# Kernel tuning notes

Hardware: AMD Instinct MI355X
Metric: run time of the kernel (lower is better)

The kernel has to match this reference:

```python
import jax, jax.numpy as jnp
import numpy as np

B, SQ, SK, D = 8, 2048, 2048, 128


def setup_inputs() -> dict:
    key = jax.random.key(0)
    kq, kk, kv = jax.random.split(key, 3)
    Q = jax.random.normal(kq, (B, SQ, D), dtype=jnp.float32)
    K = jax.random.normal(kk, (B, SK, D), dtype=jnp.float32)
    V = jax.random.normal(kv, (B, SK, D), dtype=jnp.float32)
    return {"Q": Q, "K": K, "V": V}


def reference(Q, K, V):
    d_k = K.shape[2]  # NOTE: module divides by d_k, not sqrt(d_k)
    # scores: [B, Sq, Sk]
    scores = jnp.einsum('bqd,bkd->bqk', Q, K) / d_k
    # unconventional softmax over the batch dim (dim=0), as in the source
    attn = jax.nn.softmax(scores, axis=0)
    # output: [B, Sq, D]
    return jnp.einsum('bqk,bkd->bqd', attn, V)
```

## Files before the change

kernel.cpp:

```cpp
#include <hip/hip_runtime.h>
#include <hip/hip_bf16.h>

#define B_   8
#define SQ_  2048
#define SK_  2048
#define D_   128

typedef __attribute__((ext_vector_type(8))) _Float16 f16x8;
typedef __attribute__((ext_vector_type(4))) _Float16 f16x4;
typedef __attribute__((ext_vector_type(4))) float    f32x4;

#define QK_BSTRIDE (128 * 4 * 64 * 8)
#define VF_BSTRIDE (64 * 8 * 64 * 8)

__device__ __forceinline__ void dma16(const void* g, void* l) {
    __builtin_amdgcn_global_load_lds(
        (const __attribute__((address_space(1))) unsigned int*)g,
        (__attribute__((address_space(3))) unsigned int*)l, 16, 0, 0);
}

__global__ __launch_bounds__(256)
void qkprep(const float* __restrict__ Q, const float* __restrict__ K,
            _Float16* __restrict__ Qf, _Float16* __restrict__ Kf) {
    const float* src = blockIdx.y ? K : Q;
    _Float16*    dst = blockIdx.y ? Kf : Qf;
    int gid = blockIdx.x * 256 + threadIdx.x;
    int l  = gid & 63;
    int ks = (gid >> 6) & 3;
    int t  = (gid >> 8) & 127;
    int b  = gid >> 15;
    const float* p = src + ((size_t)b * 2048 + t * 16 + (l & 15)) * 128
                         + ks * 32 + (l >> 4) * 8;
    f32x4 a = *(const f32x4*)p;
    f32x4 c = *(const f32x4*)(p + 4);
    f16x8 r;
    r[0] = (_Float16)a[0]; r[1] = (_Float16)a[1];
    r[2] = (_Float16)a[2]; r[3] = (_Float16)a[3];
    r[4] = (_Float16)c[0]; r[5] = (_Float16)c[1];
    r[6] = (_Float16)c[2]; r[7] = (_Float16)c[3];
    *(f16x8*)(dst + (size_t)gid * 8) = r;
}

__global__ __launch_bounds__(256)
void vprep(const float* __restrict__ V, _Float16* __restrict__ Vf) {
    __shared__ _Float16 T[64][136];
    const int b  = blockIdx.y;
    const int kb = blockIdx.x;
    const int t  = threadIdx.x;
    const int row = t >> 2, c0 = (t & 3) * 32;
    const float* src = V + ((size_t)b * SK_ + kb * 64 + row) * D_ + c0;
#pragma unroll
    for (int u = 0; u < 8; ++u) {
        f32x4 v = *(const f32x4*)(src + u * 4);
        f16x4 h;
        h[0] = (_Float16)v[0]; h[1] = (_Float16)v[1];
        h[2] = (_Float16)v[2]; h[3] = (_Float16)v[3];
        *(f16x4*)&T[row][c0 + u * 4] = h;
    }
    __syncthreads();
#pragma unroll
    for (int u = 0; u < 4; ++u) {
        int s   = u * 256 + t;
        int l   = s & 63;
        int dt  = (s >> 6) & 7;
        int ktl = s >> 9;
        int hi  = l >> 4, ql = l & 15;
        f16x8 r;
#pragma unroll
        for (int j = 0; j < 8; ++j) r[j] = T[ktl * 32 + hi * 8 + j][dt * 16 + ql];
        *(f16x8*)(Vf + (((size_t)b * 64 + kb * 2 + ktl) * 8 + dt) * 512 + (size_t)l * 8) = r;
    }
}

__global__ __launch_bounds__(512)
void zred(const _Float16* __restrict__ Qf, const _Float16* __restrict__ Kf,
          _Float16* __restrict__ Pf, int nqt, int qoff16) {
    __shared__ __attribute__((aligned(16))) _Float16 E[8][64][64];
    const int bid   = blockIdx.x;
    const int qtile = bid >> 5;
    const int ktile = bid & 31;
    const int b  = threadIdx.x >> 6;
    const int l  = threadIdx.x & 63;
    const int hi = l >> 4, ql = l & 15;

    const _Float16* Qb = Qf + (size_t)b * QK_BSTRIDE;
    const _Float16* Kb = Kf + (size_t)b * QK_BSTRIDE;

    f32x4 s[4][4] = {};
#pragma unroll
    for (int ks = 0; ks < 4; ++ks) {
        f16x8 kf[4];
#pragma unroll
        for (int kk = 0; kk < 4; ++kk)
            kf[kk] = *(const f16x8*)(Kb + ((((size_t)ktile * 4 + kk) * 4 + ks) * 64 + l) * 8);
#pragma unroll
        for (int qq = 0; qq < 4; ++qq) {
            f16x8 qv = *(const f16x8*)(Qb + ((((size_t)(qoff16 + qtile * 4 + qq)) * 4 + ks) * 64 + l) * 8);
#pragma unroll
            for (int kk = 0; kk < 4; ++kk)
                s[kk][qq] = __builtin_amdgcn_mfma_f32_16x16x32_f16(kf[kk], qv, s[kk][qq], 0, 0, 0);
        }
    }

    f16x4* E4 = (f16x4*)&E[0][0][0];
#pragma unroll
    for (int kk = 0; kk < 4; ++kk)
#pragma unroll
        for (int qq = 0; qq < 4; ++qq) {
            f16x4 e;
#pragma unroll
            for (int r = 0; r < 4; ++r)
                e[r] = (_Float16)__expf(s[kk][qq][r] * 0.0078125f);
            int q = qq * 16 + ql;
            int k = kk * 16 + hi * 4;
            int g16 = ((b * 64 + q) << 3) + ((k >> 3) ^ (q & 7));
            E4[g16 * 2 + ((k >> 2) & 1)] = e;
        }
    __syncthreads();

    const int t    = threadIdx.x;
    const int ktl  = t >> 8;
    const int qq2  = (t >> 6) & 3;
    const int l2   = t & 63;
    const int hi2  = l2 >> 4, ql2 = l2 & 15;
    const int q_loc  = qq2 * 16 + ql2;
    const int k0_loc = ktl * 32 + hi2 * 8;
    const f16x8* E8  = (const f16x8*)&E[0][0][0];
    const int eidx   = (q_loc << 3) + ((k0_loc >> 3) ^ (q_loc & 7));

    f16x8 z = E8[eidx];
#pragma unroll
    for (int bb = 1; bb < 8; ++bb) z = z + E8[bb * 512 + eidx];
    float inv[8];
#pragma unroll
    for (int j = 0; j < 8; ++j) inv[j] = __builtin_amdgcn_rcpf((float)z[j]);

    const size_t pbase = (((size_t)(qtile * 4 + qq2)) * 64 + (ktile * 2 + ktl)) * 512 + (size_t)l2 * 8;
#pragma unroll
    for (int bb = 0; bb < 8; ++bb) {
        f16x8 e = E8[bb * 512 + eidx];
        f16x8 p;
#pragma unroll
        for (int j = 0; j < 8; ++j) p[j] = (_Float16)((float)e[j] * inv[j]);
        *(f16x8*)(Pf + (size_t)bb * nqt * 32768 + pbase) = p;
    }
}

__global__ __launch_bounds__(512)
void av(const _Float16* __restrict__ Pf, const _Float16* __restrict__ Vf,
        float* __restrict__ out, int nqt, int qoff) {
    __shared__ __attribute__((aligned(16))) _Float16 lds[2 * 12288];

    const int bid = blockIdx.x;
    const int b   = bid & 7;
    const int mt  = bid >> 3;
    const int w   = threadIdx.x >> 6;
    const int l   = threadIdx.x & 63;
    const int wq  = w >> 2;
    const int wd  = w & 3;
    const int hi  = l >> 4, ql = l & 15;

    const _Float16* Pb = Pf + (size_t)b * nqt * 32768;
    const _Float16* Vb = Vf + (size_t)b * VF_BSTRIDE;

#define STAGE(bufi, kt2) do {                                                  \
    _Float16* dst0 = (_Float16*)lds + (bufi) * 12288;                          \
    _Pragma("unroll")                                                          \
    for (int u = 0; u < 3; ++u) {                                              \
        int c = w * 3 + u;                                                     \
        const _Float16* srcp;                                                  \
        if (c < 8)                                                             \
            srcp = Pb + (((size_t)(mt * 4 + (c >> 1))) * 64 + ((kt2) * 2 + (c & 1))) * 512 + (size_t)l * 8; \
        else {                                                                 \
            int cv = c - 8;                                                    \
            srcp = Vb + (((size_t)((kt2) * 2 + (cv >> 3))) * 8 + (cv & 7)) * 512 + (size_t)l * 8; \
        }                                                                      \
        dma16(srcp, dst0 + c * 512);                                           \
    }                                                                          \
} while (0)

    f32x4 acc[2][2] = {};
    int cur = 0;
    STAGE(0, 0);
    for (int kt2 = 0; kt2 < 32; ++kt2) {
        if (kt2 + 1 < 32) STAGE(cur ^ 1, kt2 + 1);
        __syncthreads();
        const _Float16* Bf = (const _Float16*)lds + cur * 12288;
#pragma unroll
        for (int ktl = 0; ktl < 2; ++ktl) {
            f16x8 pfr[2], vfr[2];
#pragma unroll
            for (int i = 0; i < 2; ++i)
                pfr[i] = *(const f16x8*)(Bf + ((wq * 2 + i) * 2 + ktl) * 512 + l * 8);
#pragma unroll
            for (int j = 0; j < 2; ++j)
                vfr[j] = *(const f16x8*)(Bf + 4096 + (ktl * 8 + wd * 2 + j) * 512 + l * 8);
#pragma unroll
            for (int i = 0; i < 2; ++i)
#pragma unroll
                for (int j = 0; j < 2; ++j)
                    acc[i][j] = __builtin_amdgcn_mfma_f32_16x16x32_f16(pfr[i], vfr[j], acc[i][j], 0, 0, 0);
        }
        __syncthreads();
        cur ^= 1;
    }

    const int q0 = qoff + mt * 64 + wq * 32;
#pragma unroll
    for (int i = 0; i < 2; ++i)
#pragma unroll
        for (int j = 0; j < 2; ++j)
#pragma unroll
            for (int r = 0; r < 4; ++r)
                out[((size_t)b * SQ_ + q0 + i * 16 + hi * 4 + r) * D_ + (wd * 2 + j) * 16 + ql]
                    = acc[i][j][r];
#undef STAGE
}

extern "C" void kernel_launch(void* const* d_in, const int* in_sizes, int n_in,
                              void* d_out, int out_size, void* d_ws, size_t ws_size,
                              hipStream_t stream) {
    const float* Q = (const float*)d_in[0];
    const float* K = (const float*)d_in[1];
    const float* V = (const float*)d_in[2];
    float* out = (float*)d_out;

    _Float16* Qf = (_Float16*)d_ws;
    _Float16* Kf = Qf + (size_t)B_ * QK_BSTRIDE;
    _Float16* Vf = Kf + (size_t)B_ * QK_BSTRIDE;
    _Float16* Pf = Vf + (size_t)B_ * VF_BSTRIDE;

    size_t used  = (size_t)(12 * 1024 * 1024);
    size_t avail = ws_size > used ? (ws_size - used) / 2 : 0;
    int nq = 2048;
    while (nq > 64 && (size_t)nq * 16384 > avail) nq >>= 1;
    int nchunks = 2048 / nq;
    int nqt = nq / 16;

    qkprep<<<dim3(1024, 2), 256, 0, stream>>>(Q, K, Qf, Kf);
    vprep<<<dim3(32, B_), 256, 0, stream>>>(V, Vf);

    for (int ci = 0; ci < nchunks; ++ci) {
        int qoff = ci * nq;
        zred<<<(nq / 64) * 32, 512, 0, stream>>>(Qf, Kf, Pf, nqt, qoff >> 4);
        av<<<(nq / 64) * 8, 512, 0, stream>>>(Pf, Vf, out, nqt, qoff);
    }
}
```

Baseline: 69.17 us.

## Merge prep kernels, triple-buffer AV staging with vmcnt waits, bound zred occupancy

```diff
diff --git a/kernel.cpp b/kernel.cpp
--- a/kernel.cpp
+++ b/kernel.cpp
@@ -20,59 +20,62 @@
 }
 
 __global__ __launch_bounds__(256)
-void qkprep(const float* __restrict__ Q, const float* __restrict__ K,
-            _Float16* __restrict__ Qf, _Float16* __restrict__ Kf) {
-    const float* src = blockIdx.y ? K : Q;
-    _Float16*    dst = blockIdx.y ? Kf : Qf;
-    int gid = blockIdx.x * 256 + threadIdx.x;
-    int l  = gid & 63;
-    int ks = (gid >> 6) & 3;
-    int t  = (gid >> 8) & 127;
-    int b  = gid >> 15;
-    const float* p = src + ((size_t)b * 2048 + t * 16 + (l & 15)) * 128
-                         + ks * 32 + (l >> 4) * 8;
-    f32x4 a = *(const f32x4*)p;
-    f32x4 c = *(const f32x4*)(p + 4);
-    f16x8 r;
-    r[0] = (_Float16)a[0]; r[1] = (_Float16)a[1];
-    r[2] = (_Float16)a[2]; r[3] = (_Float16)a[3];
-    r[4] = (_Float16)c[0]; r[5] = (_Float16)c[1];
-    r[6] = (_Float16)c[2]; r[7] = (_Float16)c[3];
-    *(f16x8*)(dst + (size_t)gid * 8) = r;
-}
-
-__global__ __launch_bounds__(256)
-void vprep(const float* __restrict__ V, _Float16* __restrict__ Vf) {
+void prep(const float* __restrict__ Q, const float* __restrict__ K,
+          const float* __restrict__ V,
+          _Float16* __restrict__ Qf, _Float16* __restrict__ Kf,
+          _Float16* __restrict__ Vf) {
     __shared__ _Float16 T[64][136];
-    const int b  = blockIdx.y;
-    const int kb = blockIdx.x;
-    const int t  = threadIdx.x;
-    const int row = t >> 2, c0 = (t & 3) * 32;
-    const float* src = V + ((size_t)b * SK_ + kb * 64 + row) * D_ + c0;
-#pragma unroll
-    for (int u = 0; u < 8; ++u) {
-        f32x4 v = *(const f32x4*)(src + u * 4);
-        f16x4 h;
-        h[0] = (_Float16)v[0]; h[1] = (_Float16)v[1];
-        h[2] = (_Float16)v[2]; h[3] = (_Float16)v[3];
-        *(f16x4*)&T[row][c0 + u * 4] = h;
-    }
-    __syncthreads();
-#pragma unroll
-    for (int u = 0; u < 4; ++u) {
-        int s   = u * 256 + t;
-        int l   = s & 63;
-        int dt  = (s >> 6) & 7;
-        int ktl = s >> 9;
-        int hi  = l >> 4, ql = l & 15;
+    const int bid = blockIdx.x;
+    if (bid < 2048) {
+        const float* src = (bid >= 1024) ? K : Q;
+        _Float16*    dst = (bid >= 1024) ? Kf : Qf;
+        int gid = (bid & 1023) * 256 + threadIdx.x;
+        int l  = gid & 63;
+        int ks = (gid >> 6) & 3;
+        int t  = (gid >> 8) & 127;
+        int b  = gid >> 15;
+        const float* p = src + ((size_t)b * 2048 + t * 16 + (l & 15)) * 128
+                             + ks * 32 + (l >> 4) * 8;
+        f32x4 a = *(const f32x4*)p;
+        f32x4 c = *(const f32x4*)(p + 4);
         f16x8 r;
-#pragma unroll
-        for (int j = 0; j < 8; ++j) r[j] = T[ktl * 32 + hi * 8 + j][dt * 16 + ql];
-        *(f16x8*)(Vf + (((size_t)b * 64 + kb * 2 + ktl) * 8 + dt) * 512 + (size_t)l * 8) = r;
-    }
-}
-
-__global__ __launch_bounds__(512)
+        r[0] = (_Float16)a[0]; r[1] = (_Float16)a[1];
+        r[2] = (_Float16)a[2]; r[3] = (_Float16)a[3];
+        r[4] = (_Float16)c[0]; r[5] = (_Float16)c[1];
+        r[6] = (_Float16)c[2]; r[7] = (_Float16)c[3];
+        *(f16x8*)(dst + (size_t)gid * 8) = r;
+    } else {
+        const int vb = bid - 2048;
+        const int b  = vb >> 5;
+        const int kb = vb & 31;
+        const int t  = threadIdx.x;
+        const int row = t >> 2, c0 = (t & 3) * 32;
+        const float* src = V + ((size_t)b * SK_ + kb * 64 + row) * D_ + c0;
+#pragma unroll
+        for (int u = 0; u < 8; ++u) {
+            f32x4 v = *(const f32x4*)(src + u * 4);
+            f16x4 h;
+            h[0] = (_Float16)v[0]; h[1] = (_Float16)v[1];
+            h[2] = (_Float16)v[2]; h[3] = (_Float16)v[3];
+            *(f16x4*)&T[row][c0 + u * 4] = h;
+        }
+        __syncthreads();
+#pragma unroll
+        for (int u = 0; u < 4; ++u) {
+            int s   = u * 256 + t;
+            int l   = s & 63;
+            int dt  = (s >> 6) & 7;
+            int ktl = s >> 9;
+            int hi  = l >> 4, ql = l & 15;
+            f16x8 r;
+#pragma unroll
+            for (int j = 0; j < 8; ++j) r[j] = T[ktl * 32 + hi * 8 + j][dt * 16 + ql];
+            *(f16x8*)(Vf + (((size_t)b * 64 + kb * 2 + ktl) * 8 + dt) * 512 + (size_t)l * 8) = r;
+        }
+    }
+}
+
+__global__ __launch_bounds__(512, 4)
 void zred(const _Float16* __restrict__ Qf, const _Float16* __restrict__ Kf,
           _Float16* __restrict__ Pf, int nqt, int qoff16) {
     __shared__ __attribute__((aligned(16))) _Float16 E[8][64][64];
@@ -149,7 +152,7 @@
 __global__ __launch_bounds__(512)
 void av(const _Float16* __restrict__ Pf, const _Float16* __restrict__ Vf,
         float* __restrict__ out, int nqt, int qoff) {
-    __shared__ __attribute__((aligned(16))) _Float16 lds[2 * 12288];
+    __shared__ __attribute__((aligned(16))) _Float16 lds[3 * 12288];
 
     const int bid = blockIdx.x;
     const int b   = bid & 7;
@@ -164,7 +167,7 @@
     const _Float16* Vb = Vf + (size_t)b * VF_BSTRIDE;
 
 #define STAGE(bufi, kt2) do {                                                  \
-    _Float16* dst0 = (_Float16*)lds + (bufi) * 12288;                          \
+    _Float16* dst0 = (_Float16*)lds + (size_t)(bufi) * 12288;                  \
     _Pragma("unroll")                                                          \
     for (int u = 0; u < 3; ++u) {                                              \
         int c = w * 3 + u;                                                     \
@@ -179,30 +182,41 @@
     }                                                                          \
 } while (0)
 
+#define MFMA_PHASE(bufi) do {                                                  \
+    const _Float16* Bf = (const _Float16*)lds + (size_t)(bufi) * 12288;        \
+    _Pragma("unroll")                                                          \
+    for (int ktl = 0; ktl < 2; ++ktl) {                                        \
+        f16x8 pfr[2], vfr[2];                                                  \
+        _Pragma("unroll")                                                      \
+        for (int i = 0; i < 2; ++i)                                            \
+            pfr[i] = *(const f16x8*)(Bf + ((wq * 2 + i) * 2 + ktl) * 512 + l * 8); \
+        _Pragma("unroll")                                                      \
+        for (int j = 0; j < 2; ++j)                                            \
+            vfr[j] = *(const f16x8*)(Bf + 4096 + (ktl * 8 + wd * 2 + j) * 512 + l * 8); \
+        _Pragma("unroll")                                                      \
+        for (int i = 0; i < 2; ++i)                                            \
+            _Pragma("unroll")                                                  \
+            for (int j = 0; j < 2; ++j)                                        \
+                acc[i][j] = __builtin_amdgcn_mfma_f32_16x16x32_f16(pfr[i], vfr[j], acc[i][j], 0, 0, 0); \
+    }                                                                          \
+} while (0)
+
     f32x4 acc[2][2] = {};
-    int cur = 0;
     STAGE(0, 0);
+    STAGE(1, 1);
     for (int kt2 = 0; kt2 < 32; ++kt2) {
-        if (kt2 + 1 < 32) STAGE(cur ^ 1, kt2 + 1);
-        __syncthreads();
-        const _Float16* Bf = (const _Float16*)lds + cur * 12288;
-#pragma unroll
-        for (int ktl = 0; ktl < 2; ++ktl) {
-            f16x8 pfr[2], vfr[2];
-#pragma unroll
-            for (int i = 0; i < 2; ++i)
-                pfr[i] = *(const f16x8*)(Bf + ((wq * 2 + i) * 2 + ktl) * 512 + l * 8);
-#pragma unroll
-            for (int j = 0; j < 2; ++j)
-                vfr[j] = *(const f16x8*)(Bf + 4096 + (ktl * 8 + wd * 2 + j) * 512 + l * 8);
-#pragma unroll
-            for (int i = 0; i < 2; ++i)
-#pragma unroll
-                for (int j = 0; j < 2; ++j)
-                    acc[i][j] = __builtin_amdgcn_mfma_f32_16x16x32_f16(pfr[i], vfr[j], acc[i][j], 0, 0, 0);
-        }
-        __syncthreads();
-        cur ^= 1;
+        if (kt2 < 30) {
+            STAGE((kt2 + 2) % 3, kt2 + 2);
+            asm volatile("s_waitcnt vmcnt(6)" ::: "memory");
+        } else if (kt2 == 30) {
+            asm volatile("s_waitcnt vmcnt(3)" ::: "memory");
+        } else {
+            asm volatile("s_waitcnt vmcnt(0)" ::: "memory");
+        }
+        __builtin_amdgcn_s_barrier();
+        __builtin_amdgcn_sched_barrier(0);
+        MFMA_PHASE(kt2 % 3);
+        __builtin_amdgcn_s_barrier();
     }
 
     const int q0 = qoff + mt * 64 + wq * 32;
@@ -215,6 +229,7 @@
                 out[((size_t)b * SQ_ + q0 + i * 16 + hi * 4 + r) * D_ + (wd * 2 + j) * 16 + ql]
                     = acc[i][j][r];
 #undef STAGE
+#undef MFMA_PHASE
 }
 
 extern "C" void kernel_launch(void* const* d_in, const int* in_sizes, int n_in,
@@ -237,8 +252,7 @@
     int nchunks = 2048 / nq;
     int nqt = nq / 16;
 
-    qkprep<<<dim3(1024, 2), 256, 0, stream>>>(Q, K, Qf, Kf);
-    vprep<<<dim3(32, B_), 256, 0, stream>>>(V, Vf);
+    prep<<<2048 + 256, 256, 0, stream>>>(Q, K, V, Qf, Kf, Vf);
 
     for (int ci = 0; ci < nchunks; ++ci) {
         int qoff = ci * nq;
```

New measurement: 58.26 us. 15.8% less time.
